# Performance work log

Hardware: AMD Instinct MI355X
Metric: run time of the kernel (lower is better)

Reference implementation:

```python
import jax, jax.numpy as jnp
import numpy as np

H, N, L, BATCH = 128, 64, 4096, 8


def _make_dplr_hippo(n):
    # HiPPO-LegS -> NPLR -> DPLR diagonalization (float64 numpy, as in torch source)
    ar = np.arange(n, dtype=np.float64)
    p0 = np.sqrt(1.0 + 2.0 * ar)
    A = p0[:, None] * p0[None, :]
    A = np.tril(A) - np.diag(ar)
    nhippo = -A
    Pv = np.sqrt(ar + 0.5)
    Bv = np.sqrt(2.0 * ar + 1.0)
    S = nhippo + Pv[:, None] * Pv[None, :]
    Lambda_real = np.mean(np.diag(S)) * np.ones(n)
    Lambda_imag, V = np.linalg.eigh(S * -1j)
    V = V.astype(np.complex64)
    P = (V.conj().T @ Pv.astype(np.complex64))
    B = (V.conj().T @ Bv.astype(np.complex64))
    Lam = (Lambda_real + 1j * Lambda_imag).astype(np.complex64)
    return Lam, P, B


def _ri(x):  # complex -> [..., 2] real view (like torch.view_as_real)
    return np.stack([x.real, x.imag], axis=-1).astype(np.float32)


def setup_inputs() -> dict:
    key = jax.random.key(0)
    k_u, k_c, k_d = jax.random.split(key, 3)
    Lam, P, B = _make_dplr_hippo(N)
    Lambda_ri = np.tile(_ri(Lam)[None], (H, 1, 1))          # [H, N, 2]
    P_ri = np.tile(_ri(P)[None], (H, 1, 1))                 # [H, N, 2]
    B_ri = np.tile(_ri(B)[None], (H, 1, 1))                 # [H, N, 2]
    C_ri = jax.random.normal(k_c, (H, N, 2), dtype=jnp.float32)
    D = jax.random.normal(k_d, (H, 1), dtype=jnp.float32)
    u = jax.random.normal(k_u, (BATCH, L, H), dtype=jnp.float32)
    step = jnp.array([1.0 / L], dtype=jnp.float32)
    return {
        "u": u,
        "B_ri": jnp.asarray(B_ri),
        "C_ri": jnp.asarray(C_ri),
        "D": D,
        "Lambda_ri": jnp.asarray(Lambda_ri),
        "P_ri": jnp.asarray(P_ri),
        "step": step,
    }


def _as_c(x_ri):
    return jax.lax.complex(x_ri[..., 0], x_ri[..., 1])


def reference(u, B_ri, C_ri, D, Lambda_ri, P_ri, step):
    Bc = _as_c(B_ri)        # [H, N] complex64
    Cc = _as_c(C_ri)        # [H, N]
    Lam = _as_c(Lambda_ri)  # [H, N]
    Pc = _as_c(P_ri)        # [H, N]
    batch, seq_len, h = u.shape

    # roots of unity and bilinear-transform terms
    z = jnp.exp(-2j * jnp.pi * jnp.arange(seq_len) / seq_len)   # [L] complex64
    g = (2.0 / step).astype(jnp.complex64) * ((1.0 - z) / (1.0 + z))  # [L]
    c = 2.0 / (1.0 + z)                                          # [L]

    # Cauchy resolvent, shared by the four cauchy_dot reductions: [H, L, N]
    r = 1.0 / (g[None, :, None] - Lam[:, None, :])

    def cauchy(v):  # v: [H, N] -> [H, L]
        return jnp.einsum("hn,hln->hl", v, r)

    k00 = cauchy(jnp.conj(Cc) * Bc)
    k01 = cauchy(jnp.conj(Cc) * Pc)
    k10 = cauchy(jnp.conj(Pc) * Bc)
    k11 = cauchy(jnp.conj(Pc) * Pc)
    at_roots = c[None, :] * (k00 - k01 * (1.0 / (1.0 + k11)) * k10)  # [H, L]

    kernel = jnp.fft.ifft(at_roots, n=seq_len, axis=-1).real  # [H, L] float32

    # linear (full) FFT convolution, length 2L-1, keep first L samples
    nfft = 2 * seq_len - 1
    u_f = jnp.fft.rfft(u, n=nfft, axis=1)                 # [B, F, H]
    k_f = jnp.fft.rfft(kernel, n=nfft, axis=-1)           # [H, F]
    y = jnp.fft.irfft(u_f * k_f.T[None], n=nfft, axis=1)[:, :seq_len, :]  # [B, L, H]

    return y + u @ D  # D: [H,1] -> broadcast add of skip term
```

## Files before the change

### kernel.cpp

```cpp
#include <hip/hip_runtime.h>
#include <hip/hip_bf16.h>
#include <math.h>

#define HH 128
#define NN 64
#define LL 4096
#define BB 8
#define NFFT 8192
#define KSTR 4160

#define CAU_BLOCKS 1024
#define TRU_BLOCKS 4096
#define SKP_BLOCKS 8192

__device__ __forceinline__ float2 cmul(float2 a, float2 b) {
    return make_float2(a.x * b.x - a.y * b.y, a.x * b.y + a.y * b.x);
}
__device__ __forceinline__ float2 cadd(float2 a, float2 b) {
    return make_float2(a.x + b.x, a.y + b.y);
}
__device__ __forceinline__ float2 csub(float2 a, float2 b) {
    return make_float2(a.x - b.x, a.y - b.y);
}
__device__ __forceinline__ int brev13(int x) { return (int)(__brev((unsigned)x) >> 19); }
__device__ __forceinline__ int kkmap(int t) {
    return (t < 4096) ? (((t & 63) << 6) | (t >> 6)) : 4096;
}

__device__ __forceinline__ float2 twid(float rev, float sg) {
    return make_float2(__builtin_amdgcn_cosf(rev), sg * __builtin_amdgcn_sinf(rev));
}


template <int M>
__device__ __forceinline__ void dif_f4(float2* d, int N, int tid, int nt, float sg) {
    const float inv2m = 1.0f / (2.0f * (float)M);
    const float inv4m = 1.0f / (4.0f * (float)M);
    for (int q = tid; q < (N >> 2); q += nt) {
        int j = q & (M - 1);
        int i0 = ((q & ~(M - 1)) << 2) + j;
        float2 x0 = d[i0], x1 = d[i0 + M], x2 = d[i0 + 2 * M], x3 = d[i0 + 3 * M];
        float jf = (float)j;
        float2 wB = twid(jf * inv4m, sg);
        float2 wA = twid(jf * inv2m, sg);
        float2 a0 = cadd(x0, x2);
        float2 a2 = cmul(wB, csub(x0, x2));
        float2 a1 = cadd(x1, x3);
        float2 t = cmul(wB, csub(x1, x3));
        float2 a3 = make_float2(-sg * t.y, sg * t.x);
        d[i0] = cadd(a0, a1);
        d[i0 + M] = cmul(wA, csub(a0, a1));
        d[i0 + 2 * M] = cadd(a2, a3);
        d[i0 + 3 * M] = cmul(wA, csub(a2, a3));
    }
    __syncthreads();
}

template <int M>
__device__ __forceinline__ void dit_f4(float2* d, int N, int tid, int nt, float sg) {
    const float inv2m = 1.0f / (2.0f * (float)M);
    const float inv4m = 1.0f / (4.0f * (float)M);
    for (int q = tid; q < (N >> 2); q += nt) {
        int j = q & (M - 1);
        int i0 = ((q & ~(M - 1)) << 2) + j;
        float2 x0 = d[i0], x1 = d[i0 + M], x2 = d[i0 + 2 * M], x3 = d[i0 + 3 * M];
        float jf = (float)j;
        float2 wA = twid(jf * inv2m, sg);
        float2 wB = twid(jf * inv4m, sg);
        float2 t0 = cmul(wA, x1), t1 = cmul(wA, x3);
        float2 a0 = cadd(x0, t0), a1 = csub(x0, t0);
        float2 a2 = cadd(x2, t1), a3 = csub(x2, t1);
        float2 u = cmul(wB, a2), v = cmul(wB, a3);
        float2 vi = make_float2(-sg * v.y, sg * v.x);
        d[i0] = cadd(a0, u);
        d[i0 + 2 * M] = csub(a0, u);
        d[i0 + M] = cadd(a1, vi);
        d[i0 + 3 * M] = csub(a1, vi);
    }
    __syncthreads();
}

__global__ __launch_bounds__(256, 8) void stage1_kernel(
    const float* __restrict__ u,
    const float* __restrict__ B_ri, const float* __restrict__ C_ri,
    const float* __restrict__ D,
    const float* __restrict__ Lambda_ri, const float* __restrict__ P_ri,
    const float* __restrict__ step,
    float2* __restrict__ at_g, float* __restrict__ ut, float* __restrict__ skip) {
    __shared__ float4 smem4[264];
    const int bid = blockIdx.x;
    const int tid = threadIdx.x;

    if (bid < CAU_BLOCKS) {
        const int h = bid >> 3;
        if (tid < NN) {
            int n = tid;
            float2 C = ((const float2*)C_ri)[h * NN + n];
            float2 Bv = ((const float2*)B_ri)[h * NN + n];
            float2 P = ((const float2*)P_ri)[h * NN + n];
            float2 lam = ((const float2*)Lambda_ri)[h * NN + n];
            float2 Cc = make_float2(C.x, -C.y);
            float2 Pc = make_float2(P.x, -P.y);
            float2 v00 = cmul(Cc, Bv);
            float2 v01 = cmul(Cc, P);
            float2 v10 = cmul(Pc, Bv);
            float2 v11 = cmul(Pc, P);
            smem4[n * 3 + 0] = make_float4(lam.x, lam.y, v00.x, v00.y);
            smem4[n * 3 + 1] = make_float4(v01.x, v01.y, v10.x, v10.y);
            smem4[n * 3 + 2] = make_float4(v11.x, v11.y, 0.f, 0.f);
        }
        __syncthreads();

        const int lbase = ((bid & 7) << 8) | tid;
        const float two_over_step = 2.0f / step[0];
        float gr[2], gi[2], ccx[2], ccy[2];
#pragma unroll
        for (int p = 0; p < 2; ++p) {
            int l = lbase + p * 2048;
            double th = -6.283185307179586476925286766559 * (double)l / (double)LL;
            float sn, cs;
            sincosf((float)th, &sn, &cs);
            float dr = 1.0f + cs, di = sn;
            float inv = __builtin_amdgcn_rcpf(dr * dr + di * di);
            float nr = 1.0f - cs, ni = -sn;
            gr[p] = two_over_step * (nr * dr + ni * di) * inv;
            gi[p] = two_over_step * (ni * dr - nr * di) * inv;
            ccx[p] = 2.0f * dr * inv;
            ccy[p] = -2.0f * di * inv;
        }

        float2 k00[2], k01[2], k10[2], k11[2];
#pragma unroll
        for (int p = 0; p < 2; ++p) {
            k00[p] = make_float2(0.f, 0.f);
            k01[p] = make_float2(0.f, 0.f);
            k10[p] = make_float2(0.f, 0.f);
            k11[p] = make_float2(0.f, 0.f);
        }
#pragma unroll 4
        for (int n = 0; n < NN; ++n) {
            float4 tA = smem4[n * 3 + 0];
            float4 tB = smem4[n * 3 + 1];
            float4 tC = smem4[n * 3 + 2];
#pragma unroll
            for (int p = 0; p < 2; ++p) {
                float ar = gr[p] - tA.x, ai = gi[p] - tA.y;
                float id = __builtin_amdgcn_rcpf(ar * ar + ai * ai);
                float2 r = make_float2(ar * id, -ai * id);
                k00[p] = cadd(k00[p], cmul(make_float2(tA.z, tA.w), r));
                k01[p] = cadd(k01[p], cmul(make_float2(tB.x, tB.y), r));
                k10[p] = cadd(k10[p], cmul(make_float2(tB.z, tB.w), r));
                k11[p] = cadd(k11[p], cmul(make_float2(tC.x, tC.y), r));
            }
        }
#pragma unroll
        for (int p = 0; p < 2; ++p) {
            float wr = 1.0f + k11[p].x, wi = k11[p].y;
            float iw = __builtin_amdgcn_rcpf(wr * wr + wi * wi);
            float2 winv = make_float2(wr * iw, -wi * iw);
            float2 t = cmul(cmul(k01[p], winv), k10[p]);
            float2 at = cmul(make_float2(ccx[p], ccy[p]),
                             make_float2(k00[p].x - t.x, k00[p].y - t.y));
            at_g[(size_t)h * LL + lbase + p * 2048] = at;
        }
    } else if (bid < CAU_BLOCKS + TRU_BLOCKS) {
        float* tile = (float*)smem4;
        int tb = bid - CAU_BLOCKS;
        int b = tb >> 9;
        int h0 = ((tb >> 7) & 3) * 32;
        int l0 = (tb & 127) * 32;
        int tx = tid & 31, ty = tid >> 5;
        const float* up = u + (size_t)b * LL * HH;
        float* utp = ut + (size_t)b * HH * LL;
        for (int i = ty; i < 32; i += 8)
            tile[i * 33 + tx] = up[(size_t)(l0 + i) * HH + h0 + tx];
        __syncthreads();
        for (int i = ty; i < 32; i += 8)
            utp[(size_t)(h0 + i) * LL + l0 + tx] = tile[tx * 33 + i];
    } else {
        int sb = bid - (CAU_BLOCKS + TRU_BLOCKS);
        int wid = tid >> 6, lane = tid & 63;
        int row = sb * 4 + wid;
        const float* ur = u + (size_t)row * HH;
        float v = ur[lane] * D[lane] + ur[lane + 64] * D[lane + 64];
        for (int off = 32; off > 0; off >>= 1) v += __shfl_down(v, off, 64);
        if (lane == 0) skip[row] = v;
    }
}

__global__ __launch_bounds__(1024) void kfreq_kernel(const float2* __restrict__ at_g,
                                                     float2* __restrict__ KfP) {
    __shared__ float2 sm[NFFT];
    const int h = blockIdx.x;
    const int tid = threadIdx.x;
    const float2* ap = at_g + (size_t)h * LL;
#pragma unroll
    for (int it = 0; it < 4; ++it) {
        int t = tid + it * 1024;
        int l = ((t & 63) << 6) | (t >> 6);
        sm[__brev((unsigned)l) >> 20] = ap[l];
    }
    __syncthreads();

    dit_f4<1>(sm, 4096, tid, 1024, +1.f);
    dit_f4<4>(sm, 4096, tid, 1024, +1.f);
    dit_f4<16>(sm, 4096, tid, 1024, +1.f);
    dit_f4<64>(sm, 4096, tid, 1024, +1.f);
    dit_f4<256>(sm, 4096, tid, 1024, +1.f);
    dit_f4<1024>(sm, 4096, tid, 1024, +1.f);

    const float inv8192 = 1.0f / 8192.0f;
    for (int t = tid; t < 4096; t += 1024) {
        float kv = sm[t].x * (1.0f / 4096.0f);
        float2 w = twid((float)t * inv8192, -1.f);
        sm[t] = make_float2(kv, 0.f);
        sm[t + 4096] = make_float2(kv * w.x, kv * w.y);
    }
    __syncthreads();

    dif_f4<1024>(sm, 8192, tid, 1024, -1.f);
    dif_f4<256>(sm, 8192, tid, 1024, -1.f);
    dif_f4<64>(sm, 8192, tid, 1024, -1.f);
    dif_f4<16>(sm, 8192, tid, 1024, -1.f);
    dif_f4<4>(sm, 8192, tid, 1024, -1.f);
    dif_f4<1>(sm, 8192, tid, 1024, -1.f);

    float2* kfp = KfP + (size_t)h * KSTR;
    for (int t = tid; t <= 4096; t += 1024) kfp[t] = sm[brev13(kkmap(t))];
}

__global__ __launch_bounds__(1024) void conv_fft_kernel(const float* __restrict__ ut,
                                                        const float2* __restrict__ KfP,
                                                        float* __restrict__ yt) {
    __shared__ float2 sm[NFFT];
    const int b = blockIdx.x >> 6;
    const int c = blockIdx.x & 63;
    const int h0 = 2 * c, h1 = 2 * c + 1;
    const int tid = threadIdx.x;
    const float* up0 = ut + ((size_t)b * HH + h0) * LL;
    const float* up1 = ut + ((size_t)b * HH + h1) * LL;
    const float inv8192 = 1.0f / 8192.0f;

    for (int i = tid; i < 4096; i += 1024) {
        float2 a = make_float2(up0[i], up1[i]);
        float2 w = twid((float)i * inv8192, -1.f);
        sm[i] = a;
        sm[i + 4096] = cmul(w, a);
    }
    __syncthreads();

    dif_f4<1024>(sm, 8192, tid, 1024, -1.f);
    dif_f4<256>(sm, 8192, tid, 1024, -1.f);
    dif_f4<64>(sm, 8192, tid, 1024, -1.f);
    dif_f4<16>(sm, 8192, tid, 1024, -1.f);
    dif_f4<4>(sm, 8192, tid, 1024, -1.f);
    dif_f4<1>(sm, 8192, tid, 1024, -1.f);

    const float2* kf0 = KfP + (size_t)h0 * KSTR;
    const float2* kf1 = KfP + (size_t)h1 * KSTR;
    for (int t = tid; t <= 4096; t += 1024) {
        int kk = kkmap(t);
        bool self = (kk == 0) || (kk == 4096);
        int p = brev13(kk);
        int q = self ? p : brev13(NFFT - kk);
        float2 K0 = kf0[t];
        float2 K1 = kf1[t];
        float2 Zp = sm[p];
        float2 Zq = sm[q];
        float2 U0 = make_float2(0.5f * (Zp.x + Zq.x), 0.5f * (Zp.y - Zq.y));
        float2 U1 = make_float2(0.5f * (Zp.y + Zq.y), 0.5f * (Zq.x - Zp.x));
        float2 A = cmul(U0, K0);
        float2 C = cmul(U1, K1);
        sm[p] = make_float2(A.x - C.y, A.y + C.x);
        if (!self) sm[q] = make_float2(A.x + C.y, C.x - A.y);
    }
    __syncthreads();

    dit_f4<1>(sm, 8192, tid, 1024, +1.f);
    dit_f4<4>(sm, 8192, tid, 1024, +1.f);
    dit_f4<16>(sm, 8192, tid, 1024, +1.f);
    dit_f4<64>(sm, 8192, tid, 1024, +1.f);
    dit_f4<256>(sm, 8192, tid, 1024, +1.f);
    dit_f4<1024>(sm, 8192, tid, 1024, +1.f);

    float* yp0 = yt + ((size_t)b * HH + h0) * LL;
    float* yp1 = yt + ((size_t)b * HH + h1) * LL;
    const float invN = 1.0f / (float)NFFT;
    for (int x = tid; x < 4096; x += 1024) {
        float2 w = twid((float)x * inv8192, +1.f);
        float2 a = sm[x];
        float2 bb = cmul(w, sm[x + 4096]);
        yp0[x] = (a.x + bb.x) * invN;
        yp1[x] = (a.y + bb.y) * invN;
    }
}

__global__ __launch_bounds__(256) void transpose_y_kernel(const float* __restrict__ yt,
                                                          const float* __restrict__ skip,
                                                          float* __restrict__ y) {
    __shared__ float tile[32][33];
    int b = blockIdx.z;
    int h0 = blockIdx.x * 32, l0 = blockIdx.y * 32;
    const float* ytp = yt + (size_t)b * HH * LL;
    const float* skp = skip + (size_t)b * LL;
    float* yp = y + (size_t)b * LL * HH;
    for (int i = threadIdx.y; i < 32; i += 8)
        tile[i][threadIdx.x] = ytp[(size_t)(h0 + i) * LL + l0 + threadIdx.x];
    __syncthreads();
    for (int i = threadIdx.y; i < 32; i += 8) {
        size_t idx = (size_t)(l0 + i) * HH + h0 + threadIdx.x;
        yp[idx] = tile[threadIdx.x][i] + skp[l0 + i];
    }
}

extern "C" void kernel_launch(void* const* d_in, const int* in_sizes, int n_in,
                              void* d_out, int out_size, void* d_ws, size_t ws_size,
                              hipStream_t stream) {
    const float* u = (const float*)d_in[0];
    const float* B_ri = (const float*)d_in[1];
    const float* C_ri = (const float*)d_in[2];
    const float* D = (const float*)d_in[3];
    const float* Lambda_ri = (const float*)d_in[4];
    const float* P_ri = (const float*)d_in[5];
    const float* step = (const float*)d_in[6];
    float* out = (float*)d_out;

    char* ws = (char*)d_ws;
    float2* KfP = (float2*)ws;
    float* skip = (float*)(ws + (size_t)6 * 1024 * 1024);
    float* ut = (float*)(ws + (size_t)8 * 1024 * 1024);
    float* yt = (float*)(ws + (size_t)24 * 1024 * 1024);
    float2* at_g = (float2*)yt;

    stage1_kernel<<<dim3(CAU_BLOCKS + TRU_BLOCKS + SKP_BLOCKS), dim3(256), 0, stream>>>(
        u, B_ri, C_ri, D, Lambda_ri, P_ri, step, at_g, ut, skip);
    kfreq_kernel<<<dim3(HH), dim3(1024), 0, stream>>>(at_g, KfP);
    conv_fft_kernel<<<dim3(BB * HH / 2), dim3(1024), 0, stream>>>(ut, KfP, yt);
    transpose_y_kernel<<<dim3(HH / 32, LL / 32, BB), dim3(32, 8), 0, stream>>>(yt, skip, out);
}
```

Before: 91.96 us.

## Switch shared-memory FFTs to radix-8 passes with XOR-swizzled LDS indexing

Replaces the radix-4 DIF/DIT butterfly passes with radix-8 passes, cutting the number of shared-memory round trips and barriers per FFT (6 to 4 for 4096 and 8192 points). An XOR swizzle on LDS indices is added to every shared-memory access to reduce bank conflicts from strided butterfly accesses. Radix-8 raises register pressure per thread and with 1024 threads per block some loops now leave threads idle (4096/8 = 512 work items), and extra twiddle multiplies are added.

```diff
diff --git a/kernel.cpp b/kernel.cpp
--- a/kernel.cpp
+++ b/kernel.cpp
@@ -26,6 +26,7 @@
 __device__ __forceinline__ int kkmap(int t) {
     return (t < 4096) ? (((t & 63) << 6) | (t >> 6)) : 4096;
 }
+__device__ __forceinline__ int swz(int v) { return v ^ ((v >> 4) & 15); }
 
 __device__ __forceinline__ float2 twid(float rev, float sg) {
     return make_float2(__builtin_amdgcn_cosf(rev), sg * __builtin_amdgcn_sinf(rev));
@@ -33,49 +34,93 @@
 
 
 template <int M>
-__device__ __forceinline__ void dif_f4(float2* d, int N, int tid, int nt, float sg) {
+__device__ __forceinline__ void dif_f8(float2* d, int N, int tid, int nt, float sg) {
     const float inv2m = 1.0f / (2.0f * (float)M);
     const float inv4m = 1.0f / (4.0f * (float)M);
-    for (int q = tid; q < (N >> 2); q += nt) {
+    const float inv8m = 1.0f / (8.0f * (float)M);
+    const float s2 = 0.70710678118654752f;
+    for (int q = tid; q < (N >> 3); q += nt) {
         int j = q & (M - 1);
-        int i0 = ((q & ~(M - 1)) << 2) + j;
-        float2 x0 = d[i0], x1 = d[i0 + M], x2 = d[i0 + 2 * M], x3 = d[i0 + 3 * M];
+        int i0 = ((q & ~(M - 1)) << 3) + j;
+        float2 x0 = d[swz(i0)],         x1 = d[swz(i0 + M)],
+               x2 = d[swz(i0 + 2 * M)], x3 = d[swz(i0 + 3 * M)],
+               x4 = d[swz(i0 + 4 * M)], x5 = d[swz(i0 + 5 * M)],
+               x6 = d[swz(i0 + 6 * M)], x7 = d[swz(i0 + 7 * M)];
         float jf = (float)j;
-        float2 wB = twid(jf * inv4m, sg);
-        float2 wA = twid(jf * inv2m, sg);
-        float2 a0 = cadd(x0, x2);
-        float2 a2 = cmul(wB, csub(x0, x2));
-        float2 a1 = cadd(x1, x3);
-        float2 t = cmul(wB, csub(x1, x3));
-        float2 a3 = make_float2(-sg * t.y, sg * t.x);
-        d[i0] = cadd(a0, a1);
-        d[i0 + M] = cmul(wA, csub(a0, a1));
-        d[i0 + 2 * M] = cadd(a2, a3);
-        d[i0 + 3 * M] = cmul(wA, csub(a2, a3));
+        float2 w8 = twid(jf * inv8m, sg);
+        float2 w4 = twid(jf * inv4m, sg);
+        float2 w2 = twid(jf * inv2m, sg);
+        float2 e1 = make_float2(s2, sg * s2);
+        float2 e3 = make_float2(-s2, sg * s2);
+        float2 y0 = cadd(x0, x4), y1 = cadd(x1, x5), y2 = cadd(x2, x6), y3 = cadd(x3, x7);
+        float2 t0 = csub(x0, x4), t1 = csub(x1, x5), t2 = csub(x2, x6), t3 = csub(x3, x7);
+        float2 w8i = make_float2(-sg * w8.y, sg * w8.x);
+        float2 z0 = cmul(w8, t0);
+        float2 z1 = cmul(cmul(w8, e1), t1);
+        float2 z2 = cmul(w8i, t2);
+        float2 z3 = cmul(cmul(w8, e3), t3);
+        {
+            float2 a0 = cadd(y0, y2);
+            float2 a2 = cmul(w4, csub(y0, y2));
+            float2 a1 = cadd(y1, y3);
+            float2 t = cmul(w4, csub(y1, y3));
+            float2 a3 = make_float2(-sg * t.y, sg * t.x);
+            d[swz(i0)]         = cadd(a0, a1);
+            d[swz(i0 + M)]     = cmul(w2, csub(a0, a1));
+            d[swz(i0 + 2 * M)] = cadd(a2, a3);
+            d[swz(i0 + 3 * M)] = cmul(w2, csub(a2, a3));
+        }
+        {
+            float2 a0 = cadd(z0, z2);
+            float2 a2 = cmul(w4, csub(z0, z2));
+            float2 a1 = cadd(z1, z3);
+            float2 t = cmul(w4, csub(z1, z3));
+            float2 a3 = make_float2(-sg * t.y, sg * t.x);
+            d[swz(i0 + 4 * M)] = cadd(a0, a1);
+            d[swz(i0 + 5 * M)] = cmul(w2, csub(a0, a1));
+            d[swz(i0 + 6 * M)] = cadd(a2, a3);
+            d[swz(i0 + 7 * M)] = cmul(w2, csub(a2, a3));
+        }
     }
     __syncthreads();
 }
 
 template <int M>
-__device__ __forceinline__ void dit_f4(float2* d, int N, int tid, int nt, float sg) {
+__device__ __forceinline__ void dit_f8(float2* d, int N, int tid, int nt, float sg) {
     const float inv2m = 1.0f / (2.0f * (float)M);
     const float inv4m = 1.0f / (4.0f * (float)M);
-    for (int q = tid; q < (N >> 2); q += nt) {
+    const float inv8m = 1.0f / (8.0f * (float)M);
+    const float s2 = 0.70710678118654752f;
+    for (int q = tid; q < (N >> 3); q += nt) {
         int j = q & (M - 1);
-        int i0 = ((q & ~(M - 1)) << 2) + j;
-        float2 x0 = d[i0], x1 = d[i0 + M], x2 = d[i0 + 2 * M], x3 = d[i0 + 3 * M];
+        int i0 = ((q & ~(M - 1)) << 3) + j;
+        float2 x0 = d[swz(i0)],         x1 = d[swz(i0 + M)],
+               x2 = d[swz(i0 + 2 * M)], x3 = d[swz(i0 + 3 * M)],
+               x4 = d[swz(i0 + 4 * M)], x5 = d[swz(i0 + 5 * M)],
+               x6 = d[swz(i0 + 6 * M)], x7 = d[swz(i0 + 7 * M)];
         float jf = (float)j;
         float2 wA = twid(jf * inv2m, sg);
         float2 wB = twid(jf * inv4m, sg);
-        float2 t0 = cmul(wA, x1), t1 = cmul(wA, x3);
-        float2 a0 = cadd(x0, t0), a1 = csub(x0, t0);
-        float2 a2 = cadd(x2, t1), a3 = csub(x2, t1);
-        float2 u = cmul(wB, a2), v = cmul(wB, a3);
-        float2 vi = make_float2(-sg * v.y, sg * v.x);
-        d[i0] = cadd(a0, u);
-        d[i0 + 2 * M] = csub(a0, u);
-        d[i0 + M] = cadd(a1, vi);
-        d[i0 + 3 * M] = csub(a1, vi);
+        float2 wC = twid(jf * inv8m, sg);
+        float2 t;
+        t = cmul(wA, x1); float2 b0 = cadd(x0, t), b1 = csub(x0, t);
+        t = cmul(wA, x3); float2 b2 = cadd(x2, t), b3 = csub(x2, t);
+        t = cmul(wA, x5); float2 b4 = cadd(x4, t), b5 = csub(x4, t);
+        t = cmul(wA, x7); float2 b6 = cadd(x6, t), b7 = csub(x6, t);
+        float2 wBi = make_float2(-sg * wB.y, sg * wB.x);
+        t = cmul(wB, b2);  float2 c0 = cadd(b0, t), c2 = csub(b0, t);
+        t = cmul(wBi, b3); float2 c1 = cadd(b1, t), c3 = csub(b1, t);
+        t = cmul(wB, b6);  float2 c4 = cadd(b4, t), c6 = csub(b4, t);
+        t = cmul(wBi, b7); float2 c5 = cadd(b5, t), c7 = csub(b5, t);
+        float2 e1 = make_float2(s2, sg * s2);
+        float2 e3 = make_float2(-s2, sg * s2);
+        float2 w1 = cmul(wC, e1);
+        float2 w2_ = make_float2(-sg * wC.y, sg * wC.x);
+        float2 w3 = cmul(wC, e3);
+        t = cmul(wC, c4);  d[swz(i0)]         = cadd(c0, t); d[swz(i0 + 4 * M)] = csub(c0, t);
+        t = cmul(w1, c5);  d[swz(i0 + M)]     = cadd(c1, t); d[swz(i0 + 5 * M)] = csub(c1, t);
+        t = cmul(w2_, c6); d[swz(i0 + 2 * M)] = cadd(c2, t); d[swz(i0 + 6 * M)] = csub(c2, t);
+        t = cmul(w3, c7);  d[swz(i0 + 3 * M)] = cadd(c3, t); d[swz(i0 + 7 * M)] = csub(c3, t);
     }
     __syncthreads();
 }
@@ -198,35 +243,31 @@
     for (int it = 0; it < 4; ++it) {
         int t = tid + it * 1024;
         int l = ((t & 63) << 6) | (t >> 6);
-        sm[__brev((unsigned)l) >> 20] = ap[l];
-    }
-    __syncthreads();
-
-    dit_f4<1>(sm, 4096, tid, 1024, +1.f);
-    dit_f4<4>(sm, 4096, tid, 1024, +1.f);
-    dit_f4<16>(sm, 4096, tid, 1024, +1.f);
-    dit_f4<64>(sm, 4096, tid, 1024, +1.f);
-    dit_f4<256>(sm, 4096, tid, 1024, +1.f);
-    dit_f4<1024>(sm, 4096, tid, 1024, +1.f);
+        sm[swz((int)(__brev((unsigned)l) >> 20))] = ap[l];
+    }
+    __syncthreads();
+
+    dit_f8<1>(sm, 4096, tid, 1024, +1.f);
+    dit_f8<8>(sm, 4096, tid, 1024, +1.f);
+    dit_f8<64>(sm, 4096, tid, 1024, +1.f);
+    dit_f8<512>(sm, 4096, tid, 1024, +1.f);
 
     const float inv8192 = 1.0f / 8192.0f;
     for (int t = tid; t < 4096; t += 1024) {
-        float kv = sm[t].x * (1.0f / 4096.0f);
+        float kv = sm[swz(t)].x * (1.0f / 4096.0f);
         float2 w = twid((float)t * inv8192, -1.f);
-        sm[t] = make_float2(kv, 0.f);
-        sm[t + 4096] = make_float2(kv * w.x, kv * w.y);
-    }
-    __syncthreads();
-
-    dif_f4<1024>(sm, 8192, tid, 1024, -1.f);
-    dif_f4<256>(sm, 8192, tid, 1024, -1.f);
-    dif_f4<64>(sm, 8192, tid, 1024, -1.f);
-    dif_f4<16>(sm, 8192, tid, 1024, -1.f);
-    dif_f4<4>(sm, 8192, tid, 1024, -1.f);
-    dif_f4<1>(sm, 8192, tid, 1024, -1.f);
+        sm[swz(t)] = make_float2(kv, 0.f);
+        sm[swz(t + 4096)] = make_float2(kv * w.x, kv * w.y);
+    }
+    __syncthreads();
+
+    dif_f8<512>(sm, 8192, tid, 1024, -1.f);
+    dif_f8<64>(sm, 8192, tid, 1024, -1.f);
+    dif_f8<8>(sm, 8192, tid, 1024, -1.f);
+    dif_f8<1>(sm, 8192, tid, 1024, -1.f);
 
     float2* kfp = KfP + (size_t)h * KSTR;
-    for (int t = tid; t <= 4096; t += 1024) kfp[t] = sm[brev13(kkmap(t))];
+    for (int t = tid; t <= 4096; t += 1024) kfp[t] = sm[swz(brev13(kkmap(t)))];
 }
 
 __global__ __launch_bounds__(1024) void conv_fft_kernel(const float* __restrict__ ut,
@@ -244,25 +285,23 @@
     for (int i = tid; i < 4096; i += 1024) {
         float2 a = make_float2(up0[i], up1[i]);
         float2 w = twid((float)i * inv8192, -1.f);
-        sm[i] = a;
-        sm[i + 4096] = cmul(w, a);
-    }
-    __syncthreads();
-
-    dif_f4<1024>(sm, 8192, tid, 1024, -1.f);
-    dif_f4<256>(sm, 8192, tid, 1024, -1.f);
-    dif_f4<64>(sm, 8192, tid, 1024, -1.f);
-    dif_f4<16>(sm, 8192, tid, 1024, -1.f);
-    dif_f4<4>(sm, 8192, tid, 1024, -1.f);
-    dif_f4<1>(sm, 8192, tid, 1024, -1.f);
+        sm[swz(i)] = a;
+        sm[swz(i + 4096)] = cmul(w, a);
+    }
+    __syncthreads();
+
+    dif_f8<512>(sm, 8192, tid, 1024, -1.f);
+    dif_f8<64>(sm, 8192, tid, 1024, -1.f);
+    dif_f8<8>(sm, 8192, tid, 1024, -1.f);
+    dif_f8<1>(sm, 8192, tid, 1024, -1.f);
 
     const float2* kf0 = KfP + (size_t)h0 * KSTR;
     const float2* kf1 = KfP + (size_t)h1 * KSTR;
     for (int t = tid; t <= 4096; t += 1024) {
         int kk = kkmap(t);
         bool self = (kk == 0) || (kk == 4096);
-        int p = brev13(kk);
-        int q = self ? p : brev13(NFFT - kk);
+        int p = swz(brev13(kk));
+        int q = self ? p : swz(brev13(NFFT - kk));
         float2 K0 = kf0[t];
         float2 K1 = kf1[t];
         float2 Zp = sm[p];
@@ -276,20 +315,18 @@
     }
     __syncthreads();
 
-    dit_f4<1>(sm, 8192, tid, 1024, +1.f);
-    dit_f4<4>(sm, 8192, tid, 1024, +1.f);
-    dit_f4<16>(sm, 8192, tid, 1024, +1.f);
-    dit_f4<64>(sm, 8192, tid, 1024, +1.f);
-    dit_f4<256>(sm, 8192, tid, 1024, +1.f);
-    dit_f4<1024>(sm, 8192, tid, 1024, +1.f);
+    dit_f8<1>(sm, 8192, tid, 1024, +1.f);
+    dit_f8<8>(sm, 8192, tid, 1024, +1.f);
+    dit_f8<64>(sm, 8192, tid, 1024, +1.f);
+    dit_f8<512>(sm, 8192, tid, 1024, +1.f);
 
     float* yp0 = yt + ((size_t)b * HH + h0) * LL;
     float* yp1 = yt + ((size_t)b * HH + h1) * LL;
     const float invN = 1.0f / (float)NFFT;
     for (int x = tid; x < 4096; x += 1024) {
         float2 w = twid((float)x * inv8192, +1.f);
-        float2 a = sm[x];
-        float2 bb = cmul(w, sm[x + 4096]);
+        float2 a = sm[swz(x)];
+        float2 bb = cmul(w, sm[swz(x + 4096)]);
         yp0[x] = (a.x + bb.x) * invN;
         yp1[x] = (a.y + bb.y) * invN;
     }
```

Result: faster. 83.43 us (-9.3%).
